# Kernel tuning notes

Hardware: AMD Instinct MI355X
Metric: run time of the kernel (lower is better)

The kernel has to match this reference:

```python
import jax, jax.numpy as jnp
import numpy as np

B, NPG, K, H, G, L = 8, 128, 64, 600, 50, 6
N = B * NPG
CUTOFF = 10.0
BOX = 20.0
NUM_Z = 100


def setup_inputs() -> dict:
    key = jax.random.key(0)
    ks = jax.random.split(key, 16)
    s = 0.05
    z = jax.random.randint(ks[0], (N,), 0, 85)
    pos = jax.random.uniform(ks[1], (N, 3), dtype=jnp.float32) * BOX
    # weights stored as [in, out] (transposed torch Linear) so x @ w applies directly
    inp = {
        "z": z,
        "pos": pos,
        "embedding": jax.random.normal(ks[2], (NUM_Z, H), jnp.float32) * s,
        "mlp_w1": jax.random.normal(ks[3], (L, G, H), jnp.float32) * s,
        "mlp_b1": jnp.zeros((L, H), jnp.float32),
        "mlp_w2": jax.random.normal(ks[4], (L, H, H), jnp.float32) * s,
        "mlp_b2": jnp.zeros((L, H), jnp.float32),
        "lin1_w": jax.random.normal(ks[5], (L, H, H), jnp.float32) * s,  # CFConv lin1, no bias
        "lin2_w": jax.random.normal(ks[6], (L, H, H), jnp.float32) * s,
        "lin2_b": jnp.zeros((L, H), jnp.float32),
        "int_lin_w": jax.random.normal(ks[7], (L, H, H), jnp.float32) * s,
        "int_lin_b": jnp.zeros((L, H), jnp.float32),
        "pool_w": jax.random.normal(ks[8], (H, H), jnp.float32) * s,
        "pool_b": jnp.zeros((H,), jnp.float32),
    }
    return inp


def _ssp(x):
    # shifted softplus used by SchNet
    return jax.nn.softplus(x) - jnp.log(2.0)


def _build_graph(pos):
    # radius graph within each of the B graphs, capped at K neighbors per node
    posg = pos.reshape(B, NPG, 3)
    diff = posg[:, :, None, :] - posg[:, None, :, :]          # [B,n,n,3]
    dist2 = jnp.sum(diff * diff, axis=-1)                     # [B,n,n]
    eye = jnp.eye(NPG, dtype=bool)
    ok = (dist2 <= CUTOFF * CUTOFF) & (~eye)[None]
    neg = jnp.where(ok, -dist2, -jnp.inf)
    vals, idx = jax.lax.top_k(neg, K)                         # nearest K in-radius
    valid = jnp.isfinite(vals)                                # [B,n,K]
    nbr = idx + (jnp.arange(B) * NPG)[:, None, None]          # global node ids
    # recompute distances from gathered positions (differentiable, safe at masked slots)
    pos_nbr = pos[nbr.reshape(-1)].reshape(B, NPG, K, 3)
    dvec = posg[:, :, None, :] - pos_nbr
    dsq = jnp.sum(dvec * dvec, axis=-1)
    d = jnp.sqrt(jnp.where(valid, dsq, 1.0))
    d = jnp.where(valid, d, 0.0)                              # [B,n,K]
    return nbr, d, valid.astype(pos.dtype)


def reference(pos, embedding, mlp_w1, mlp_b1, mlp_w2, mlp_b2, lin1_w, lin2_w,
              lin2_b, int_lin_w, int_lin_b, pool_w, pool_b, z):
    nbr, d, valid = _build_graph(pos)
    nbr_flat = nbr.reshape(-1)

    # Gaussian smearing
    offs = jnp.linspace(0.0, CUTOFF, G)
    coeff = -0.5 / (offs[1] - offs[0]) ** 2
    edge_attr = jnp.exp(coeff * (d[..., None] - offs) ** 2)   # [B,n,K,G]
    # cosine cutoff, zero for invalid (padded) edges
    C = 0.5 * (jnp.cos(d * jnp.pi / CUTOFF) + 1.0) * valid    # [B,n,K]

    h = embedding[z]                                          # [N,H]
    for l in range(L):
        Wf = _ssp(edge_attr @ mlp_w1[l] + mlp_b1[l]) @ mlp_w2[l] + mlp_b2[l]
        Wf = Wf * C[..., None]                                # [B,n,K,H]
        x1 = h @ lin1_w[l]                                    # [N,H]
        xj = x1[nbr_flat].reshape(B, NPG, K, H)               # gather neighbors
        msg = jnp.sum(xj * Wf, axis=2).reshape(N, H)          # aggregate (add)
        m = msg @ lin2_w[l] + lin2_b[l]
        m = _ssp(m)
        m = m @ int_lin_w[l] + int_lin_b[l]
        h = h + m

    pooled = h.reshape(B, NPG, H).mean(axis=1)                # mean pool per graph
    return pooled @ pool_w + pool_b                           # [B, emb_dim]
```

## Files before the change

### kernel.cpp

```cpp
#include <hip/hip_runtime.h>
#include <cmath>

#define NB   8
#define NPG  128
#define NN   1024
#define KNB  64
#define HD   600
#define GG   50
#define LL   6
#define EE   (NN*KNB)
#define WROW 640
#define WCOL 608
#define NKNOT 1024

typedef __attribute__((ext_vector_type(8))) short short8;
typedef __attribute__((ext_vector_type(4))) short short4v;
typedef __attribute__((ext_vector_type(4))) float f32x4;

__device__ __forceinline__ short f2b(float f) {
  union { float f; unsigned u; } v; v.f = f;
  unsigned u = v.u;
  u += 0x7fffu + ((u >> 16) & 1u);
  return (short)(u >> 16);
}

__device__ __forceinline__ float b2f(unsigned us) {
  union { unsigned u; float f; } v; v.u = us << 16; return v.f;
}

__device__ __forceinline__ float ssp_fast(float x) {
  return fmaxf(x, 0.0f) + __logf(1.0f + __expf(-fabsf(x))) - 0.69314718055994531f;
}

__global__ __launch_bounds__(128) void build_graph_k(const float* __restrict__ pos,
        int* __restrict__ nbr, float* __restrict__ dist, float* __restrict__ cval) {
#pragma clang fp contract(off)
  __shared__ float d2s[128];
  __shared__ int scnt;
  int i = blockIdx.x;
  int li = i & 127;
  int base = i - li;
  int j = threadIdx.x;
  if (j == 0) scnt = 0;
  float px = pos[3*i], py = pos[3*i+1], pz = pos[3*i+2];
  int gj = base + j;
  float dx = px - pos[3*gj], dy = py - pos[3*gj+1], dz = pz - pos[3*gj+2];
  float d2 = dx*dx + dy*dy + dz*dz;
  bool valid = (j != li) && (d2 <= 100.0f);
  d2s[j] = valid ? d2 : 3.0e38f;
  __syncthreads();
  if (valid) {
    atomicAdd(&scnt, 1);
    int rank = 0;
    for (int j2 = 0; j2 < 128; ++j2) {
      float o = d2s[j2];
      rank += (o < d2 || (o == d2 && j2 < j)) ? 1 : 0;
    }
    if (rank < KNB) {
      int e = i*KNB + rank;
      nbr[e] = gj;
      float d = sqrtf(d2);
      dist[e] = d;
      cval[e] = 0.5f * (cosf(d * 0.31415926535897931f) + 1.0f);
    }
  }
  __syncthreads();
  int cnt = scnt; if (cnt > KNB) cnt = KNB;
  if (j < KNB && j >= cnt) {
    int e = i*KNB + j;
    nbr[e] = i; dist[e] = 0.0f; cval[e] = 0.0f;
  }
}

__global__ __launch_bounds__(256) void prep_k(const float* __restrict__ w1,
    short* __restrict__ basis, short* __restrict__ w1b) {
  int idx = blockIdx.x*256 + threadIdx.x;
  if (idx < NKNOT*64) {
    int i = idx >> 6, g = idx & 63;
    float v = 0.0f;
    if (g < GG) {
      const float step = 10.0f/49.0f;
      const float coeff = -0.5f/(step*step);
      float d = (float)i * (10.0f/(float)(NKNOT-1));
      float dd = d - step*(float)g;
      v = __expf(coeff*dd*dd);
    }
    basis[idx] = f2b(v);
  } else {
    int r = idx - NKNOT*64;
    if (r >= LL*WROW*64) return;
    int l = r / (WROW*64); int rem = r - l*WROW*64;
    int n = rem >> 6, k = rem & 63;
    float v = (n < HD && k < GG) ? w1[(size_t)l*GG*HD + (size_t)k*HD + n] : 0.0f;
    w1b[r] = f2b(v);
  }
}

__global__ __launch_bounds__(256) void conv_all_k(const float* __restrict__ l1w,
    const float* __restrict__ l2w, const float* __restrict__ ilw,
    const float* __restrict__ w2, short* __restrict__ dst) {
  __shared__ float T[64][65];
  int w = blockIdx.x;
  int kind = w / 6, l = w - kind*6;
  const float* s = (kind == 0) ? l1w : (kind == 1) ? l2w : (kind == 2) ? ilw : w2;
  s += (size_t)l*360000;
  int n0 = blockIdx.y*64, k0 = blockIdx.z*64;
  int tid = threadIdx.x;
  int ta = tid & 63, tb = tid >> 6;
  #pragma unroll
  for (int p = 0; p < 16; ++p) {
    int k = k0 + p*4 + tb;
    int n = n0 + ta;
    T[p*4 + tb][ta] = (k < HD && n < HD) ? s[(size_t)k*HD + n] : 0.0f;
  }
  __syncthreads();
  #pragma unroll
  for (int p = 0; p < 16; ++p) {
    int n = n0 + p*4 + tb;
    int k = k0 + ta;
    if (k < WCOL)
      dst[(size_t)w*WROW*WCOL + (size_t)n*WCOL + k] = f2b(T[ta][p*4 + tb]);
  }
}

__global__ __launch_bounds__(256) void embed_k(const int* __restrict__ z,
        const float* __restrict__ emb, float* __restrict__ h, short* __restrict__ hb) {
  int i = blockIdx.x;
  int zi = z[i];
  for (int j = threadIdx.x; j < WCOL; j += 256) {
    float v = (j < HD) ? emb[(size_t)zi*HD + j] : 0.0f;
    if (j < HD) h[(size_t)i*HD + j] = v;
    hb[(size_t)i*WCOL + j] = f2b(v);
  }
}

__global__ __launch_bounds__(256) void tabA_k(const short* __restrict__ basis,
    const short* __restrict__ w1b, const float* __restrict__ b1all,
    short* __restrict__ ttab_all) {
  const int MT = NKNOT/128;
  int l = blockIdx.x / MT;
  int mb = blockIdx.x - l*MT;
  const short* Bw = w1b + (size_t)l*WROW*64;
  short* outb = ttab_all + (size_t)l*NKNOT*WCOL;
  __shared__ __align__(16) short As[128*40];
  __shared__ __align__(16) short Bs[128*40];
  int tid = threadIdx.x;
  int lane = tid & 63, wv = tid >> 6;
  int wr = wv >> 1, wc = wv & 1;
  int col = lane & 15, quad = lane >> 4;
  int m0 = mb * 128;
  int n0 = blockIdx.y * 128;
  f32x4 acc[4][4] = {};
  for (int k0 = 0; k0 < 64; k0 += 32) {
    #pragma unroll
    for (int rep = 0; rep < 2; ++rep) {
      int s = tid + rep*256;
      int row = s >> 2, seg = s & 3;
      *(short8*)&As[row*40 + seg*8] =
          *(const short8*)(basis + (size_t)(m0 + row)*64 + k0 + seg*8);
      *(short8*)&Bs[row*40 + seg*8] =
          *(const short8*)(Bw + (size_t)(n0 + row)*64 + k0 + seg*8);
    }
    __syncthreads();
    short8 af[4], bf[4];
    #pragma unroll
    for (int mt = 0; mt < 4; ++mt)
      af[mt] = *(const short8*)&As[(wr*64 + mt*16 + col)*40 + quad*8];
    #pragma unroll
    for (int jt = 0; jt < 4; ++jt)
      bf[jt] = *(const short8*)&Bs[(wc*64 + jt*16 + col)*40 + quad*8];
    #pragma unroll
    for (int mt = 0; mt < 4; ++mt)
      #pragma unroll
      for (int jt = 0; jt < 4; ++jt)
        acc[mt][jt] = __builtin_amdgcn_mfma_f32_16x16x32_bf16(af[mt], bf[jt], acc[mt][jt], 0, 0, 0);
    __syncthreads();
  }
  #pragma unroll
  for (int jt = 0; jt < 4; ++jt) {
    int j = n0 + wc*64 + jt*16 + col;
    if (j >= WCOL) continue;
    float bj = (j < HD) ? b1all[(size_t)l*HD + j] : 0.0f;
    #pragma unroll
    for (int mt = 0; mt < 4; ++mt)
      #pragma unroll
      for (int r = 0; r < 4; ++r) {
        int row = m0 + wr*64 + mt*16 + quad*4 + r;
        short v = (j < HD) ? f2b(ssp_fast(acc[mt][jt][r] + bj)) : (short)0;
        outb[(size_t)row*WCOL + j] = v;
      }
  }
}

__global__ __launch_bounds__(256) void tabB_k(const short* __restrict__ ttab_all,
    const short* __restrict__ nwall, const float* __restrict__ b2all,
    short* __restrict__ wtab_b) {
  const int MT = NKNOT/128;
  int l = blockIdx.x / MT;
  int mb = blockIdx.x - l*MT;
  const short* A  = ttab_all + (size_t)l*NKNOT*WCOL;
  const short* Bw = nwall + (size_t)(18 + l)*WROW*WCOL;
  short* P = wtab_b + (size_t)l*NKNOT*HD;
  __shared__ __align__(16) short As[128*40];
  __shared__ __align__(16) short Bs[128*40];
  int tid = threadIdx.x;
  int lane = tid & 63, wv = tid >> 6;
  int wr = wv >> 1, wc = wv & 1;
  int col = lane & 15, quad = lane >> 4;
  int m0 = mb * 128;
  int n0 = blockIdx.y * 128;
  f32x4 acc[4][4] = {};
  for (int k0 = 0; k0 < WCOL; k0 += 32) {
    #pragma unroll
    for (int rep = 0; rep < 2; ++rep) {
      int s = tid + rep*256;
      int row = s >> 2, seg = s & 3;
      *(short8*)&As[row*40 + seg*8] =
          *(const short8*)(A + (size_t)(m0 + row)*WCOL + k0 + seg*8);
      *(short8*)&Bs[row*40 + seg*8] =
          *(const short8*)(Bw + (size_t)(n0 + row)*WCOL + k0 + seg*8);
    }
    __syncthreads();
    short8 af[4], bf[4];
    #pragma unroll
    for (int mt = 0; mt < 4; ++mt)
      af[mt] = *(const short8*)&As[(wr*64 + mt*16 + col)*40 + quad*8];
    #pragma unroll
    for (int jt = 0; jt < 4; ++jt)
      bf[jt] = *(const short8*)&Bs[(wc*64 + jt*16 + col)*40 + quad*8];
    #pragma unroll
    for (int mt = 0; mt < 4; ++mt)
      #pragma unroll
      for (int jt = 0; jt < 4; ++jt)
        acc[mt][jt] = __builtin_amdgcn_mfma_f32_16x16x32_bf16(af[mt], bf[jt], acc[mt][jt], 0, 0, 0);
    __syncthreads();
  }
  #pragma unroll
  for (int jt = 0; jt < 4; ++jt) {
    int j = n0 + wc*64 + jt*16 + col;
    if (j >= HD) continue;
    float bj = b2all[(size_t)l*HD + j];
    #pragma unroll
    for (int mt = 0; mt < 4; ++mt)
      #pragma unroll
      for (int r = 0; r < 4; ++r) {
        int row = m0 + wr*64 + mt*16 + quad*4 + r;
        P[(size_t)row*HD + j] = f2b(acc[mt][jt][r] + bj);
      }
  }
}

__global__ __launch_bounds__(192) void gather_k(const short* __restrict__ tabb,
    const float* __restrict__ cval, const int* __restrict__ nbr,
    const float* __restrict__ dist, const short* __restrict__ x1b,
    short* __restrict__ msgb) {
  __shared__ float cvs[64];
  __shared__ int nbs[64];
  __shared__ int tix[64];
  __shared__ float tfr[64];
  int node = blockIdx.x, tid = threadIdx.x;
  if (tid < 64) {
    int e = node*KNB + tid;
    cvs[tid] = cval[e];
    nbs[tid] = nbr[e];
    float u = dist[e] * ((float)(NKNOT-1)/10.0f);
    int i = (int)u;
    if (i > NKNOT-2) i = NKNOT-2;
    tix[tid] = i;
    tfr[tid] = u - (float)i;
  }
  __syncthreads();
  int j = tid*4;
  if (j >= WCOL) return;
  if (j >= HD) {
    *(uint2*)&msgb[(size_t)node*WCOL + j] = make_uint2(0u, 0u);
    return;
  }
  float s[4] = {0.f, 0.f, 0.f, 0.f};
  #pragma unroll 4
  for (int e = 0; e < KNB; ++e) {
    float Ce = cvs[e];
    if (Ce == 0.0f) continue;
    const short* w0 = tabb + (size_t)tix[e]*HD + j;
    float f = tfr[e];
    uint2 wa = *(const uint2*)w0;
    uint2 wb = *(const uint2*)(w0 + HD);
    uint2 xv = *(const uint2*)(x1b + (size_t)nbs[e]*WCOL + j);
    float a0 = b2f(wa.x & 0xffffu), a1 = b2f(wa.x >> 16);
    float a2 = b2f(wa.y & 0xffffu), a3 = b2f(wa.y >> 16);
    float b0 = b2f(wb.x & 0xffffu), b1 = b2f(wb.x >> 16);
    float b2v = b2f(wb.y & 0xffffu), b3 = b2f(wb.y >> 16);
    float x0 = b2f(xv.x & 0xffffu), x1v = b2f(xv.x >> 16);
    float x2 = b2f(xv.y & 0xffffu), x3 = b2f(xv.y >> 16);
    s[0] += Ce * (a0 + f*(b0 - a0)) * x0;
    s[1] += Ce * (a1 + f*(b1 - a1)) * x1v;
    s[2] += Ce * (a2 + f*(b2v - a2)) * x2;
    s[3] += Ce * (a3 + f*(b3 - a3)) * x3;
  }
  uint2 pack;
  pack.x = (unsigned)(unsigned short)f2b(s[0]) | ((unsigned)(unsigned short)f2b(s[1]) << 16);
  pack.y = (unsigned)(unsigned short)f2b(s[2]) | ((unsigned)(unsigned short)f2b(s[3]) << 16);
  *(uint2*)&msgb[(size_t)node*WCOL + j] = pack;
}

template<int MODE>
__global__ __launch_bounds__(256) void gemm_node_k(
    const short* __restrict__ A, const short* __restrict__ Bw,
    const float* __restrict__ bias, float* __restrict__ outf,
    short* __restrict__ outb, float* __restrict__ hacc) {
  __shared__ __align__(16) short As[2][32*40];
  __shared__ __align__(16) short Bs[2][64*40];
  int tid = threadIdx.x;
  int lane = tid & 63, wv = tid >> 6;
  int col = lane & 15, quad = lane >> 4;
  int m0 = blockIdx.x * 32;
  int n0 = blockIdx.y * 64;
  int ar = tid >> 3, aseg = tid & 7;
  int br = tid >> 2, bseg = tid & 3;
  const short* Aptr = A  + (size_t)(m0 + ar)*WCOL + aseg*4;
  const short* Bptr = Bw + (size_t)(n0 + br)*WCOL + bseg*8;
  f32x4 acc[2] = {};
  {
    short4v a0 = *(const short4v*)Aptr;
    short8  b0 = *(const short8*)Bptr;
    *(short4v*)&As[0][ar*40 + aseg*4] = a0;
    *(short8*)&Bs[0][br*40 + bseg*8] = b0;
  }
  __syncthreads();
  for (int kk = 0; kk < 19; ++kk) {
    int cur = kk & 1, nxt = cur ^ 1;
    short4v a_n; short8 b_n;
    if (kk < 18) {
      a_n = *(const short4v*)(Aptr + (kk + 1)*32);
      b_n = *(const short8*) (Bptr + (kk + 1)*32);
    }
    short8 bf = *(const short8*)&Bs[cur][(wv*16 + col)*40 + quad*8];
    #pragma unroll
    for (int mt = 0; mt < 2; ++mt) {
      short8 af = *(const short8*)&As[cur][(mt*16 + col)*40 + quad*8];
      acc[mt] = __builtin_amdgcn_mfma_f32_16x16x32_bf16(af, bf, acc[mt], 0, 0, 0);
    }
    if (kk < 18) {
      *(short4v*)&As[nxt][ar*40 + aseg*4] = a_n;
      *(short8*)&Bs[nxt][br*40 + bseg*8] = b_n;
    }
    __syncthreads();
  }
  int j = n0 + wv*16 + col;
  if (MODE == 0) {
    if (j < WCOL) {
      #pragma unroll
      for (int mt = 0; mt < 2; ++mt)
        #pragma unroll
        for (int r = 0; r < 4; ++r) {
          int row = m0 + mt*16 + quad*4 + r;
          outb[(size_t)row*WCOL + j] = (j < HD) ? f2b(acc[mt][r]) : (short)0;
        }
    }
  } else if (MODE == 1) {
    if (j < WCOL) {
      float bj = (j < HD) ? bias[j] : 0.0f;
      #pragma unroll
      for (int mt = 0; mt < 2; ++mt)
        #pragma unroll
        for (int r = 0; r < 4; ++r) {
          int row = m0 + mt*16 + quad*4 + r;
          outb[(size_t)row*WCOL + j] = (j < HD) ? f2b(ssp_fast(acc[mt][r] + bj)) : (short)0;
        }
    }
  } else {
    if (j < WCOL) {
      #pragma unroll
      for (int mt = 0; mt < 2; ++mt)
        #pragma unroll
        for (int r = 0; r < 4; ++r) {
          int row = m0 + mt*16 + quad*4 + r;
          if (j < HD) {
            float nv = hacc[(size_t)row*HD + j] + acc[mt][r] + bias[j];
            hacc[(size_t)row*HD + j] = nv;
            outb[(size_t)row*WCOL + j] = f2b(nv);
          } else {
            outb[(size_t)row*WCOL + j] = 0;
          }
        }
    }
  }
}

__global__ __launch_bounds__(256) void pool_mean_k(const float* __restrict__ h,
                                                   float* __restrict__ pooled) {
  int b = blockIdx.x;
  int c = blockIdx.y*256 + threadIdx.x;
  if (c >= HD) return;
  float s = 0.0f;
  for (int n = 0; n < NPG; ++n) s += h[(size_t)(b*NPG + n)*HD + c];
  pooled[(size_t)b*HD + c] = s * (1.0f/128.0f);
}

__global__ __launch_bounds__(256) void pool_out_k(const float* __restrict__ pooled,
    const float* __restrict__ pw, const float* __restrict__ pb,
    float* __restrict__ out) {
  __shared__ float red[4][64];
  int b = blockIdx.y;
  int tid = threadIdx.x;
  int jl = tid & 63, q = tid >> 6;
  int j = blockIdx.x*64 + jl;
  float s = 0.0f;
  if (j < HD) {
    int c0 = q*150, c1 = c0 + 150;
    for (int c = c0; c < c1; ++c)
      s += pooled[(size_t)b*HD + c] * pw[(size_t)c*HD + j];
  }
  red[q][jl] = s;
  __syncthreads();
  if (q == 0 && j < HD)
    out[(size_t)b*HD + j] = red[0][jl] + red[1][jl] + red[2][jl] + red[3][jl] + pb[j];
}

extern "C" void kernel_launch(void* const* d_in, const int* in_sizes, int n_in,
                              void* d_out, int out_size, void* d_ws, size_t ws_size,
                              hipStream_t stream) {
  const int*   z    = (const int*)d_in[0];
  const float* pos  = (const float*)d_in[1];
  const float* emb  = (const float*)d_in[2];
  const float* w1   = (const float*)d_in[3];
  const float* b1   = (const float*)d_in[4];
  const float* w2   = (const float*)d_in[5];
  const float* b2   = (const float*)d_in[6];
  const float* l1w  = (const float*)d_in[7];
  const float* l2w  = (const float*)d_in[8];
  const float* l2b  = (const float*)d_in[9];
  const float* ilw  = (const float*)d_in[10];
  const float* ilb  = (const float*)d_in[11];
  const float* pw   = (const float*)d_in[12];
  const float* pb   = (const float*)d_in[13];
  float* ws = (float*)d_ws;
  int*   nbr   = (int*)ws;
  float* cv    = ws + 65536;
  float* dist  = ws + 131072;
  float* pooled= ws + 196608;
  float* h     = ws + 204800;
  short* h_b   = (short*)(ws + 819200);
  short* msg_b = (short*)(ws + 1130496);
  short* mtmp_b= (short*)(ws + 1441792);
  short* x1_b  = (short*)(ws + 1753088);
  short* basis = (short*)(ws + 2064384);
  short* ttab  = (short*)(ws + 2097152);
  short* wtab_b= (short*)(ws + 3964928);
  short* w1b   = (short*)(ws + 5808128);
  short* nwall = (short*)(ws + 5931008);
  float* out   = (float*)d_out;

  const size_t WSZ = (size_t)WROW*WCOL;

  build_graph_k<<<NN, 128, 0, stream>>>(pos, nbr, dist, cv);
  prep_k<<<(NKNOT*64 + LL*WROW*64 + 255)/256, 256, 0, stream>>>(w1, basis, w1b);
  conv_all_k<<<dim3(24, 10, 10), 256, 0, stream>>>(l1w, l2w, ilw, w2, nwall);
  embed_k<<<NN, 256, 0, stream>>>(z, emb, h, h_b);

  tabA_k<<<dim3(LL*(NKNOT/128), 5), 256, 0, stream>>>(basis, w1b, b1, ttab);
  tabB_k<<<dim3(LL*(NKNOT/128), 5), 256, 0, stream>>>(ttab, nwall, b2, wtab_b);

  dim3 gn(32, 10);
  for (int l = 0; l < LL; ++l) {
    gemm_node_k<0><<<gn, 256, 0, stream>>>(h_b, nwall + (size_t)(0*6 + l)*WSZ,
        nullptr, nullptr, x1_b, nullptr);
    gather_k<<<NN, 192, 0, stream>>>(wtab_b + (size_t)l*NKNOT*HD, cv, nbr, dist, x1_b, msg_b);
    gemm_node_k<1><<<gn, 256, 0, stream>>>(msg_b, nwall + (size_t)(1*6 + l)*WSZ,
        l2b + (size_t)l*HD, nullptr, mtmp_b, nullptr);
    gemm_node_k<2><<<gn, 256, 0, stream>>>(mtmp_b, nwall + (size_t)(2*6 + l)*WSZ,
        ilb + (size_t)l*HD, nullptr, h_b, h);
  }
  pool_mean_k<<<dim3(NB, 3), 256, 0, stream>>>(h, pooled);
  pool_out_k<<<dim3(10, NB), 256, 0, stream>>>(pooled, pw, pb, out);
}
```

Before: 501.8 us.

## Fuse per-layer GEMM/gather launches into one cooperative persistent kernel

Replaces the 24 per-layer launches plus two pooling launches with a single cooperative kernel of 256 blocks that loops over tiles and nodes and separates stages with grid-wide barriers. The aim is to remove kernel launch and inter-kernel drain gaps. In exchange it adds grid.sync costs and fixes the block count, so gather nodes and GEMM tiles are strided over fewer resident blocks. A fallback multi-launch path remains if the cooperative launch fails.

```diff
diff --git a/kernel.cpp b/kernel.cpp
--- a/kernel.cpp
+++ b/kernel.cpp
@@ -1,5 +1,8 @@
 #include <hip/hip_runtime.h>
+#include <hip/hip_cooperative_groups.h>
 #include <cmath>
+
+namespace cg = cooperative_groups;
 
 #define NB   8
 #define NPG  128
@@ -12,6 +15,8 @@
 #define WROW 640
 #define WCOL 608
 #define NKNOT 1024
+#define GRIDB 256
+#define NTILE 320
 
 typedef __attribute__((ext_vector_type(8))) short short8;
 typedef __attribute__((ext_vector_type(4))) short short4v;
@@ -250,15 +255,94 @@
   }
 }
 
-__global__ __launch_bounds__(192) void gather_k(const short* __restrict__ tabb,
-    const float* __restrict__ cval, const int* __restrict__ nbr,
-    const float* __restrict__ dist, const short* __restrict__ x1b,
-    short* __restrict__ msgb) {
-  __shared__ float cvs[64];
-  __shared__ int nbs[64];
-  __shared__ int tix[64];
-  __shared__ float tfr[64];
-  int node = blockIdx.x, tid = threadIdx.x;
+template<int MODE>
+__device__ __forceinline__ void gemm_stage(int bx, int by,
+    const short* __restrict__ A, const short* __restrict__ Bw,
+    const float* __restrict__ bias, short* __restrict__ outb,
+    float* __restrict__ hacc, short* AsB, short* BsB) {
+  int tid = threadIdx.x;
+  int lane = tid & 63, wv = tid >> 6;
+  int col = lane & 15, quad = lane >> 4;
+  int m0 = bx * 32;
+  int n0 = by * 64;
+  int ar = tid >> 3, aseg = tid & 7;
+  int br = tid >> 2, bseg = tid & 3;
+  const short* Aptr = A  + (size_t)(m0 + ar)*WCOL + aseg*4;
+  const short* Bptr = Bw + (size_t)(n0 + br)*WCOL + bseg*8;
+  f32x4 acc[2] = {};
+  {
+    short4v a0 = *(const short4v*)Aptr;
+    short8  b0 = *(const short8*)Bptr;
+    *(short4v*)&AsB[0*32*40 + ar*40 + aseg*4] = a0;
+    *(short8*)&BsB[0*64*40 + br*40 + bseg*8] = b0;
+  }
+  __syncthreads();
+  for (int kk = 0; kk < 19; ++kk) {
+    int cur = kk & 1, nxt = cur ^ 1;
+    short4v a_n; short8 b_n;
+    if (kk < 18) {
+      a_n = *(const short4v*)(Aptr + (kk + 1)*32);
+      b_n = *(const short8*) (Bptr + (kk + 1)*32);
+    }
+    short8 bf = *(const short8*)&BsB[cur*64*40 + (wv*16 + col)*40 + quad*8];
+    #pragma unroll
+    for (int mt = 0; mt < 2; ++mt) {
+      short8 af = *(const short8*)&AsB[cur*32*40 + (mt*16 + col)*40 + quad*8];
+      acc[mt] = __builtin_amdgcn_mfma_f32_16x16x32_bf16(af, bf, acc[mt], 0, 0, 0);
+    }
+    if (kk < 18) {
+      *(short4v*)&AsB[nxt*32*40 + ar*40 + aseg*4] = a_n;
+      *(short8*)&BsB[nxt*64*40 + br*40 + bseg*8] = b_n;
+    }
+    __syncthreads();
+  }
+  int j = n0 + wv*16 + col;
+  if (MODE == 0) {
+    if (j < WCOL) {
+      #pragma unroll
+      for (int mt = 0; mt < 2; ++mt)
+        #pragma unroll
+        for (int r = 0; r < 4; ++r) {
+          int row = m0 + mt*16 + quad*4 + r;
+          outb[(size_t)row*WCOL + j] = (j < HD) ? f2b(acc[mt][r]) : (short)0;
+        }
+    }
+  } else if (MODE == 1) {
+    if (j < WCOL) {
+      float bj = (j < HD) ? bias[j] : 0.0f;
+      #pragma unroll
+      for (int mt = 0; mt < 2; ++mt)
+        #pragma unroll
+        for (int r = 0; r < 4; ++r) {
+          int row = m0 + mt*16 + quad*4 + r;
+          outb[(size_t)row*WCOL + j] = (j < HD) ? f2b(ssp_fast(acc[mt][r] + bj)) : (short)0;
+        }
+    }
+  } else {
+    if (j < WCOL) {
+      #pragma unroll
+      for (int mt = 0; mt < 2; ++mt)
+        #pragma unroll
+        for (int r = 0; r < 4; ++r) {
+          int row = m0 + mt*16 + quad*4 + r;
+          if (j < HD) {
+            float nv = hacc[(size_t)row*HD + j] + acc[mt][r] + bias[j];
+            hacc[(size_t)row*HD + j] = nv;
+            outb[(size_t)row*WCOL + j] = f2b(nv);
+          } else {
+            outb[(size_t)row*WCOL + j] = 0;
+          }
+        }
+    }
+  }
+}
+
+__device__ __forceinline__ void gather_body(int node, int tid,
+    const short* __restrict__ tabb, const float* __restrict__ cval,
+    const int* __restrict__ nbr, const float* __restrict__ dist,
+    const short* __restrict__ x1b, short* __restrict__ msgb,
+    float* cvs, int* nbs, int* tix, float* tfr) {
+  __syncthreads();
   if (tid < 64) {
     int e = node*KNB + tid;
     cvs[tid] = cval[e];
@@ -306,85 +390,23 @@
 template<int MODE>
 __global__ __launch_bounds__(256) void gemm_node_k(
     const short* __restrict__ A, const short* __restrict__ Bw,
-    const float* __restrict__ bias, float* __restrict__ outf,
-    short* __restrict__ outb, float* __restrict__ hacc) {
-  __shared__ __align__(16) short As[2][32*40];
-  __shared__ __align__(16) short Bs[2][64*40];
-  int tid = threadIdx.x;
-  int lane = tid & 63, wv = tid >> 6;
-  int col = lane & 15, quad = lane >> 4;
-  int m0 = blockIdx.x * 32;
-  int n0 = blockIdx.y * 64;
-  int ar = tid >> 3, aseg = tid & 7;
-  int br = tid >> 2, bseg = tid & 3;
-  const short* Aptr = A  + (size_t)(m0 + ar)*WCOL + aseg*4;
-  const short* Bptr = Bw + (size_t)(n0 + br)*WCOL + bseg*8;
-  f32x4 acc[2] = {};
-  {
-    short4v a0 = *(const short4v*)Aptr;
-    short8  b0 = *(const short8*)Bptr;
-    *(short4v*)&As[0][ar*40 + aseg*4] = a0;
-    *(short8*)&Bs[0][br*40 + bseg*8] = b0;
-  }
-  __syncthreads();
-  for (int kk = 0; kk < 19; ++kk) {
-    int cur = kk & 1, nxt = cur ^ 1;
-    short4v a_n; short8 b_n;
-    if (kk < 18) {
-      a_n = *(const short4v*)(Aptr + (kk + 1)*32);
-      b_n = *(const short8*) (Bptr + (kk + 1)*32);
-    }
-    short8 bf = *(const short8*)&Bs[cur][(wv*16 + col)*40 + quad*8];
-    #pragma unroll
-    for (int mt = 0; mt < 2; ++mt) {
-      short8 af = *(const short8*)&As[cur][(mt*16 + col)*40 + quad*8];
-      acc[mt] = __builtin_amdgcn_mfma_f32_16x16x32_bf16(af, bf, acc[mt], 0, 0, 0);
-    }
-    if (kk < 18) {
-      *(short4v*)&As[nxt][ar*40 + aseg*4] = a_n;
-      *(short8*)&Bs[nxt][br*40 + bseg*8] = b_n;
-    }
-    __syncthreads();
-  }
-  int j = n0 + wv*16 + col;
-  if (MODE == 0) {
-    if (j < WCOL) {
-      #pragma unroll
-      for (int mt = 0; mt < 2; ++mt)
-        #pragma unroll
-        for (int r = 0; r < 4; ++r) {
-          int row = m0 + mt*16 + quad*4 + r;
-          outb[(size_t)row*WCOL + j] = (j < HD) ? f2b(acc[mt][r]) : (short)0;
-        }
-    }
-  } else if (MODE == 1) {
-    if (j < WCOL) {
-      float bj = (j < HD) ? bias[j] : 0.0f;
-      #pragma unroll
-      for (int mt = 0; mt < 2; ++mt)
-        #pragma unroll
-        for (int r = 0; r < 4; ++r) {
-          int row = m0 + mt*16 + quad*4 + r;
-          outb[(size_t)row*WCOL + j] = (j < HD) ? f2b(ssp_fast(acc[mt][r] + bj)) : (short)0;
-        }
-    }
-  } else {
-    if (j < WCOL) {
-      #pragma unroll
-      for (int mt = 0; mt < 2; ++mt)
-        #pragma unroll
-        for (int r = 0; r < 4; ++r) {
-          int row = m0 + mt*16 + quad*4 + r;
-          if (j < HD) {
-            float nv = hacc[(size_t)row*HD + j] + acc[mt][r] + bias[j];
-            hacc[(size_t)row*HD + j] = nv;
-            outb[(size_t)row*WCOL + j] = f2b(nv);
-          } else {
-            outb[(size_t)row*WCOL + j] = 0;
-          }
-        }
-    }
-  }
+    const float* __restrict__ bias, short* __restrict__ outb,
+    float* __restrict__ hacc) {
+  __shared__ __align__(16) short AsB[2*32*40];
+  __shared__ __align__(16) short BsB[2*64*40];
+  gemm_stage<MODE>(blockIdx.x, blockIdx.y, A, Bw, bias, outb, hacc, AsB, BsB);
+}
+
+__global__ __launch_bounds__(192) void gather_k(const short* __restrict__ tabb,
+    const float* __restrict__ cval, const int* __restrict__ nbr,
+    const float* __restrict__ dist, const short* __restrict__ x1b,
+    short* __restrict__ msgb) {
+  __shared__ float cvs[64];
+  __shared__ int nbs[64];
+  __shared__ int tix[64];
+  __shared__ float tfr[64];
+  gather_body(blockIdx.x, threadIdx.x, tabb, cval, nbr, dist, x1b, msgb,
+              cvs, nbs, tix, tfr);
 }
 
 __global__ __launch_bounds__(256) void pool_mean_k(const float* __restrict__ h,
@@ -415,6 +437,74 @@
   __syncthreads();
   if (q == 0 && j < HD)
     out[(size_t)b*HD + j] = red[0][jl] + red[1][jl] + red[2][jl] + red[3][jl] + pb[j];
+}
+
+__global__ __launch_bounds__(256) void layers_k(
+    const short* __restrict__ nwall,
+    const float* __restrict__ l2b, const float* __restrict__ ilb,
+    const float* __restrict__ cv, const int* __restrict__ nbr,
+    const float* __restrict__ dist, const short* __restrict__ wtab_b,
+    float* __restrict__ h, short* __restrict__ h_b,
+    short* __restrict__ x1_b, short* __restrict__ msg_b,
+    short* __restrict__ mtmp_b, float* __restrict__ pooled,
+    const float* __restrict__ pw, const float* __restrict__ pb,
+    float* __restrict__ out) {
+  cg::grid_group grid = cg::this_grid();
+  __shared__ __align__(16) short AsB[2*32*40];
+  __shared__ __align__(16) short BsB[2*64*40];
+  __shared__ float cvs[64];
+  __shared__ int nbs[64];
+  __shared__ int tix[64];
+  __shared__ float tfr[64];
+  __shared__ float red[4][64];
+  int bid = blockIdx.x;
+  int tid = threadIdx.x;
+  const size_t WSZ = (size_t)WROW*WCOL;
+  for (int l = 0; l < LL; ++l) {
+    for (int t = bid; t < NTILE; t += GRIDB)
+      gemm_stage<0>(t & 31, t >> 5, h_b, nwall + (size_t)(0*6 + l)*WSZ,
+                    nullptr, x1_b, nullptr, AsB, BsB);
+    grid.sync();
+    {
+      const short* tabb = wtab_b + (size_t)l*NKNOT*HD;
+      for (int node = bid; node < NN; node += GRIDB)
+        gather_body(node, tid, tabb, cv, nbr, dist, x1_b, msg_b, cvs, nbs, tix, tfr);
+    }
+    grid.sync();
+    for (int t = bid; t < NTILE; t += GRIDB)
+      gemm_stage<1>(t & 31, t >> 5, msg_b, nwall + (size_t)(1*6 + l)*WSZ,
+                    l2b + (size_t)l*HD, mtmp_b, nullptr, AsB, BsB);
+    grid.sync();
+    for (int t = bid; t < NTILE; t += GRIDB)
+      gemm_stage<2>(t & 31, t >> 5, mtmp_b, nwall + (size_t)(2*6 + l)*WSZ,
+                    ilb + (size_t)l*HD, h_b, h, AsB, BsB);
+    grid.sync();
+  }
+  if (bid < 24) {
+    int b = bid & 7, cy = bid >> 3;
+    int c = cy*256 + tid;
+    if (c < HD) {
+      float s = 0.0f;
+      for (int n = 0; n < NPG; ++n) s += h[(size_t)(b*NPG + n)*HD + c];
+      pooled[(size_t)b*HD + c] = s * (1.0f/128.0f);
+    }
+  }
+  grid.sync();
+  if (bid < 80) {
+    int jx = bid % 10, b = bid / 10;
+    int jl = tid & 63, q = tid >> 6;
+    int j = jx*64 + jl;
+    float s = 0.0f;
+    if (j < HD) {
+      int c0 = q*150, c1 = c0 + 150;
+      for (int c = c0; c < c1; ++c)
+        s += pooled[(size_t)b*HD + c] * pw[(size_t)c*HD + j];
+    }
+    red[q][jl] = s;
+    __syncthreads();
+    if (q == 0 && j < HD)
+      out[(size_t)b*HD + j] = red[0][jl] + red[1][jl] + red[2][jl] + red[3][jl] + pb[j];
+  }
 }
 
 extern "C" void kernel_launch(void* const* d_in, const int* in_sizes, int n_in,
@@ -461,16 +551,27 @@
   tabA_k<<<dim3(LL*(NKNOT/128), 5), 256, 0, stream>>>(basis, w1b, b1, ttab);
   tabB_k<<<dim3(LL*(NKNOT/128), 5), 256, 0, stream>>>(ttab, nwall, b2, wtab_b);
 
-  dim3 gn(32, 10);
-  for (int l = 0; l < LL; ++l) {
-    gemm_node_k<0><<<gn, 256, 0, stream>>>(h_b, nwall + (size_t)(0*6 + l)*WSZ,
-        nullptr, nullptr, x1_b, nullptr);
-    gather_k<<<NN, 192, 0, stream>>>(wtab_b + (size_t)l*NKNOT*HD, cv, nbr, dist, x1_b, msg_b);
-    gemm_node_k<1><<<gn, 256, 0, stream>>>(msg_b, nwall + (size_t)(1*6 + l)*WSZ,
-        l2b + (size_t)l*HD, nullptr, mtmp_b, nullptr);
-    gemm_node_k<2><<<gn, 256, 0, stream>>>(mtmp_b, nwall + (size_t)(2*6 + l)*WSZ,
-        ilb + (size_t)l*HD, nullptr, h_b, h);
-  }
-  pool_mean_k<<<dim3(NB, 3), 256, 0, stream>>>(h, pooled);
-  pool_out_k<<<dim3(10, NB), 256, 0, stream>>>(pooled, pw, pb, out);
-}
+  void* args[] = {
+    (void*)&nwall, (void*)&l2b, (void*)&ilb, (void*)&cv, (void*)&nbr,
+    (void*)&dist, (void*)&wtab_b, (void*)&h, (void*)&h_b, (void*)&x1_b,
+    (void*)&msg_b, (void*)&mtmp_b, (void*)&pooled, (void*)&pw, (void*)&pb,
+    (void*)&out
+  };
+  hipError_t ce = hipLaunchCooperativeKernel((const void*)layers_k, dim3(GRIDB),
+                                             dim3(256), args, 0, stream);
+  if (ce != hipSuccess) {
+    dim3 gn(32, 10);
+    for (int l = 0; l < LL; ++l) {
+      gemm_node_k<0><<<gn, 256, 0, stream>>>(h_b, nwall + (size_t)(0*6 + l)*WSZ,
+          nullptr, x1_b, nullptr);
+      gather_k<<<NN, 192, 0, stream>>>(wtab_b + (size_t)l*NKNOT*HD, cv, nbr, dist,
+          x1_b, msg_b);
+      gemm_node_k<1><<<gn, 256, 0, stream>>>(msg_b, nwall + (size_t)(1*6 + l)*WSZ,
+          l2b + (size_t)l*HD, mtmp_b, nullptr);
+      gemm_node_k<2><<<gn, 256, 0, stream>>>(mtmp_b, nwall + (size_t)(2*6 + l)*WSZ,
+          ilb + (size_t)l*HD, h_b, h);
+    }
+    pool_mean_k<<<dim3(NB, 3), 256, 0, stream>>>(h, pooled);
+    pool_out_k<<<dim3(10, NB), 256, 0, stream>>>(pooled, pw, pb, out);
+  }
+}
```

Result: slower. 1.548 ms (+208.4%).

## Fuse filter-table GEMMs through LDS and merge pooling kernels

Applied to the files above, without the earlier changes.

Merges the two filter-table GEMM kernels into one. Each block computes a 64-row slice of the ssp(basis@W1+b1) intermediate, holds it in LDS and multiplies it by W2 straight away, so the intermediate no longer round-trips through global memory. The mean-pool and output-projection kernels are also merged, with each block recomputing the per-graph mean into shared memory. The cost is fewer, heavier blocks (96) that read weights directly from global memory without LDS staging, and redundant mean computation across blocks.

```diff
diff --git a/kernel.cpp b/kernel.cpp
--- a/kernel.cpp
+++ b/kernel.cpp
@@ -134,119 +134,85 @@
   }
 }
 
-__global__ __launch_bounds__(256) void tabA_k(const short* __restrict__ basis,
+__global__ __launch_bounds__(256) void tab_fused_k(const short* __restrict__ basis,
     const short* __restrict__ w1b, const float* __restrict__ b1all,
-    short* __restrict__ ttab_all) {
-  const int MT = NKNOT/128;
-  int l = blockIdx.x / MT;
-  int mb = blockIdx.x - l*MT;
-  const short* Bw = w1b + (size_t)l*WROW*64;
-  short* outb = ttab_all + (size_t)l*NKNOT*WCOL;
-  __shared__ __align__(16) short As[128*40];
-  __shared__ __align__(16) short Bs[128*40];
+    const short* __restrict__ nwall, const float* __restrict__ b2all,
+    short* __restrict__ wtab_b) {
+  __shared__ __align__(16) short T[64*616];
+  int blk = blockIdx.x;
+  int l = blk >> 4, rb = blk & 15;
+  int m0 = rb * 64;
+  const short* w1l = w1b + (size_t)l*WROW*64;
+  const short* w2l = nwall + (size_t)(18 + l)*WROW*WCOL;
+  short* P = wtab_b + (size_t)l*NKNOT*HD;
   int tid = threadIdx.x;
   int lane = tid & 63, wv = tid >> 6;
   int wr = wv >> 1, wc = wv & 1;
   int col = lane & 15, quad = lane >> 4;
-  int m0 = mb * 128;
-  int n0 = blockIdx.y * 128;
-  f32x4 acc[4][4] = {};
-  for (int k0 = 0; k0 < 64; k0 += 32) {
+  for (int ct = 0; ct < 10; ++ct) {
+    int n0 = ct*64;
+    f32x4 acc[2][2] = {};
     #pragma unroll
-    for (int rep = 0; rep < 2; ++rep) {
-      int s = tid + rep*256;
-      int row = s >> 2, seg = s & 3;
-      *(short8*)&As[row*40 + seg*8] =
-          *(const short8*)(basis + (size_t)(m0 + row)*64 + k0 + seg*8);
-      *(short8*)&Bs[row*40 + seg*8] =
-          *(const short8*)(Bw + (size_t)(n0 + row)*64 + k0 + seg*8);
-    }
-    __syncthreads();
-    short8 af[4], bf[4];
+    for (int k0 = 0; k0 < 64; k0 += 32) {
+      short8 af[2], bf[2];
+      #pragma unroll
+      for (int mt = 0; mt < 2; ++mt)
+        af[mt] = *(const short8*)(basis + (size_t)(m0 + wr*32 + mt*16 + col)*64 + k0 + quad*8);
+      #pragma unroll
+      for (int jt = 0; jt < 2; ++jt)
+        bf[jt] = *(const short8*)(w1l + (size_t)(n0 + wc*32 + jt*16 + col)*64 + k0 + quad*8);
+      #pragma unroll
+      for (int mt = 0; mt < 2; ++mt)
+        #pragma unroll
+        for (int jt = 0; jt < 2; ++jt)
+          acc[mt][jt] = __builtin_amdgcn_mfma_f32_16x16x32_bf16(af[mt], bf[jt], acc[mt][jt], 0, 0, 0);
+    }
     #pragma unroll
-    for (int mt = 0; mt < 4; ++mt)
-      af[mt] = *(const short8*)&As[(wr*64 + mt*16 + col)*40 + quad*8];
+    for (int jt = 0; jt < 2; ++jt) {
+      int j = n0 + wc*32 + jt*16 + col;
+      if (j >= WCOL) continue;
+      float bj = (j < HD) ? b1all[(size_t)l*HD + j] : 0.0f;
+      #pragma unroll
+      for (int mt = 0; mt < 2; ++mt)
+        #pragma unroll
+        for (int r = 0; r < 4; ++r) {
+          int row = wr*32 + mt*16 + quad*4 + r;
+          short v = (j < HD) ? f2b(ssp_fast(acc[mt][jt][r] + bj)) : (short)0;
+          T[row*616 + j] = v;
+        }
+    }
+  }
+  __syncthreads();
+  for (int ct = 0; ct < 10; ++ct) {
+    int n0 = ct*64;
+    f32x4 acc[2][2] = {};
+    for (int k0 = 0; k0 < WCOL; k0 += 32) {
+      short8 af[2], bf[2];
+      #pragma unroll
+      for (int mt = 0; mt < 2; ++mt)
+        af[mt] = *(const short8*)&T[(wr*32 + mt*16 + col)*616 + k0 + quad*8];
+      #pragma unroll
+      for (int jt = 0; jt < 2; ++jt)
+        bf[jt] = *(const short8*)(w2l + (size_t)(n0 + wc*32 + jt*16 + col)*WCOL + k0 + quad*8);
+      #pragma unroll
+      for (int mt = 0; mt < 2; ++mt)
+        #pragma unroll
+        for (int jt = 0; jt < 2; ++jt)
+          acc[mt][jt] = __builtin_amdgcn_mfma_f32_16x16x32_bf16(af[mt], bf[jt], acc[mt][jt], 0, 0, 0);
+    }
     #pragma unroll
-    for (int jt = 0; jt < 4; ++jt)
-      bf[jt] = *(const short8*)&Bs[(wc*64 + jt*16 + col)*40 + quad*8];
-    #pragma unroll
-    for (int mt = 0; mt < 4; ++mt)
-      #pragma unroll
-      for (int jt = 0; jt < 4; ++jt)
-        acc[mt][jt] = __builtin_amdgcn_mfma_f32_16x16x32_bf16(af[mt], bf[jt], acc[mt][jt], 0, 0, 0);
-    __syncthreads();
-  }
-  #pragma unroll
-  for (int jt = 0; jt < 4; ++jt) {
-    int j = n0 + wc*64 + jt*16 + col;
-    if (j >= WCOL) continue;
-    float bj = (j < HD) ? b1all[(size_t)l*HD + j] : 0.0f;
-    #pragma unroll
-    for (int mt = 0; mt < 4; ++mt)
-      #pragma unroll
-      for (int r = 0; r < 4; ++r) {
-        int row = m0 + wr*64 + mt*16 + quad*4 + r;
-        short v = (j < HD) ? f2b(ssp_fast(acc[mt][jt][r] + bj)) : (short)0;
-        outb[(size_t)row*WCOL + j] = v;
-      }
-  }
-}
-
-__global__ __launch_bounds__(256) void tabB_k(const short* __restrict__ ttab_all,
-    const short* __restrict__ nwall, const float* __restrict__ b2all,
-    short* __restrict__ wtab_b) {
-  const int MT = NKNOT/128;
-  int l = blockIdx.x / MT;
-  int mb = blockIdx.x - l*MT;
-  const short* A  = ttab_all + (size_t)l*NKNOT*WCOL;
-  const short* Bw = nwall + (size_t)(18 + l)*WROW*WCOL;
-  short* P = wtab_b + (size_t)l*NKNOT*HD;
-  __shared__ __align__(16) short As[128*40];
-  __shared__ __align__(16) short Bs[128*40];
-  int tid = threadIdx.x;
-  int lane = tid & 63, wv = tid >> 6;
-  int wr = wv >> 1, wc = wv & 1;
-  int col = lane & 15, quad = lane >> 4;
-  int m0 = mb * 128;
-  int n0 = blockIdx.y * 128;
-  f32x4 acc[4][4] = {};
-  for (int k0 = 0; k0 < WCOL; k0 += 32) {
-    #pragma unroll
-    for (int rep = 0; rep < 2; ++rep) {
-      int s = tid + rep*256;
-      int row = s >> 2, seg = s & 3;
-      *(short8*)&As[row*40 + seg*8] =
-          *(const short8*)(A + (size_t)(m0 + row)*WCOL + k0 + seg*8);
-      *(short8*)&Bs[row*40 + seg*8] =
-          *(const short8*)(Bw + (size_t)(n0 + row)*WCOL + k0 + seg*8);
-    }
-    __syncthreads();
-    short8 af[4], bf[4];
-    #pragma unroll
-    for (int mt = 0; mt < 4; ++mt)
-      af[mt] = *(const short8*)&As[(wr*64 + mt*16 + col)*40 + quad*8];
-    #pragma unroll
-    for (int jt = 0; jt < 4; ++jt)
-      bf[jt] = *(const short8*)&Bs[(wc*64 + jt*16 + col)*40 + quad*8];
-    #pragma unroll
-    for (int mt = 0; mt < 4; ++mt)
-      #pragma unroll
-      for (int jt = 0; jt < 4; ++jt)
-        acc[mt][jt] = __builtin_amdgcn_mfma_f32_16x16x32_bf16(af[mt], bf[jt], acc[mt][jt], 0, 0, 0);
-    __syncthreads();
-  }
-  #pragma unroll
-  for (int jt = 0; jt < 4; ++jt) {
-    int j = n0 + wc*64 + jt*16 + col;
-    if (j >= HD) continue;
-    float bj = b2all[(size_t)l*HD + j];
-    #pragma unroll
-    for (int mt = 0; mt < 4; ++mt)
-      #pragma unroll
-      for (int r = 0; r < 4; ++r) {
-        int row = m0 + wr*64 + mt*16 + quad*4 + r;
-        P[(size_t)row*HD + j] = f2b(acc[mt][jt][r] + bj);
-      }
+    for (int jt = 0; jt < 2; ++jt) {
+      int j = n0 + wc*32 + jt*16 + col;
+      if (j >= HD) continue;
+      float bj = b2all[(size_t)l*HD + j];
+      #pragma unroll
+      for (int mt = 0; mt < 2; ++mt)
+        #pragma unroll
+        for (int r = 0; r < 4; ++r) {
+          int row = m0 + wr*32 + mt*16 + quad*4 + r;
+          P[(size_t)row*HD + j] = f2b(acc[mt][jt][r] + bj);
+        }
+    }
   }
 }
 
@@ -306,8 +272,8 @@
 template<int MODE>
 __global__ __launch_bounds__(256) void gemm_node_k(
     const short* __restrict__ A, const short* __restrict__ Bw,
-    const float* __restrict__ bias, float* __restrict__ outf,
-    short* __restrict__ outb, float* __restrict__ hacc) {
+    const float* __restrict__ bias, short* __restrict__ outb,
+    float* __restrict__ hacc) {
   __shared__ __align__(16) short As[2][32*40];
   __shared__ __align__(16) short Bs[2][64*40];
   int tid = threadIdx.x;
@@ -387,29 +353,26 @@
   }
 }
 
-__global__ __launch_bounds__(256) void pool_mean_k(const float* __restrict__ h,
-                                                   float* __restrict__ pooled) {
-  int b = blockIdx.x;
-  int c = blockIdx.y*256 + threadIdx.x;
-  if (c >= HD) return;
-  float s = 0.0f;
-  for (int n = 0; n < NPG; ++n) s += h[(size_t)(b*NPG + n)*HD + c];
-  pooled[(size_t)b*HD + c] = s * (1.0f/128.0f);
-}
-
-__global__ __launch_bounds__(256) void pool_out_k(const float* __restrict__ pooled,
+__global__ __launch_bounds__(256) void pool_k(const float* __restrict__ h,
     const float* __restrict__ pw, const float* __restrict__ pb,
     float* __restrict__ out) {
+  __shared__ float ps[HD];
   __shared__ float red[4][64];
   int b = blockIdx.y;
   int tid = threadIdx.x;
+  for (int c = tid; c < HD; c += 256) {
+    float s = 0.0f;
+    for (int n = 0; n < NPG; ++n) s += h[(size_t)(b*NPG + n)*HD + c];
+    ps[c] = s * (1.0f/128.0f);
+  }
+  __syncthreads();
   int jl = tid & 63, q = tid >> 6;
   int j = blockIdx.x*64 + jl;
   float s = 0.0f;
   if (j < HD) {
     int c0 = q*150, c1 = c0 + 150;
     for (int c = c0; c < c1; ++c)
-      s += pooled[(size_t)b*HD + c] * pw[(size_t)c*HD + j];
+      s += ps[c] * pw[(size_t)c*HD + j];
   }
   red[q][jl] = s;
   __syncthreads();
@@ -438,14 +401,12 @@
   int*   nbr   = (int*)ws;
   float* cv    = ws + 65536;
   float* dist  = ws + 131072;
-  float* pooled= ws + 196608;
   float* h     = ws + 204800;
   short* h_b   = (short*)(ws + 819200);
   short* msg_b = (short*)(ws + 1130496);
   short* mtmp_b= (short*)(ws + 1441792);
   short* x1_b  = (short*)(ws + 1753088);
   short* basis = (short*)(ws + 2064384);
-  short* ttab  = (short*)(ws + 2097152);
   short* wtab_b= (short*)(ws + 3964928);
   short* w1b   = (short*)(ws + 5808128);
   short* nwall = (short*)(ws + 5931008);
@@ -458,19 +419,17 @@
   conv_all_k<<<dim3(24, 10, 10), 256, 0, stream>>>(l1w, l2w, ilw, w2, nwall);
   embed_k<<<NN, 256, 0, stream>>>(z, emb, h, h_b);
 
-  tabA_k<<<dim3(LL*(NKNOT/128), 5), 256, 0, stream>>>(basis, w1b, b1, ttab);
-  tabB_k<<<dim3(LL*(NKNOT/128), 5), 256, 0, stream>>>(ttab, nwall, b2, wtab_b);
+  tab_fused_k<<<LL*16, 256, 0, stream>>>(basis, w1b, b1, nwall, b2, wtab_b);
 
   dim3 gn(32, 10);
   for (int l = 0; l < LL; ++l) {
     gemm_node_k<0><<<gn, 256, 0, stream>>>(h_b, nwall + (size_t)(0*6 + l)*WSZ,
-        nullptr, nullptr, x1_b, nullptr);
+        nullptr, x1_b, nullptr);
     gather_k<<<NN, 192, 0, stream>>>(wtab_b + (size_t)l*NKNOT*HD, cv, nbr, dist, x1_b, msg_b);
     gemm_node_k<1><<<gn, 256, 0, stream>>>(msg_b, nwall + (size_t)(1*6 + l)*WSZ,
-        l2b + (size_t)l*HD, nullptr, mtmp_b, nullptr);
+        l2b + (size_t)l*HD, mtmp_b, nullptr);
     gemm_node_k<2><<<gn, 256, 0, stream>>>(mtmp_b, nwall + (size_t)(2*6 + l)*WSZ,
-        ilb + (size_t)l*HD, nullptr, h_b, h);
-  }
-  pool_mean_k<<<dim3(NB, 3), 256, 0, stream>>>(h, pooled);
-  pool_out_k<<<dim3(10, NB), 256, 0, stream>>>(pooled, pw, pb, out);
-}
+        ilb + (size_t)l*HD, h_b, h);
+  }
+  pool_k<<<dim3(10, NB), 256, 0, stream>>>(h, pw, pb, out);
+}
```

After: 538.9 us. 1.07x slower.
